# Optimization experiments

Hardware: AMD Instinct MI355X
Metric: run time of the kernel (lower is better)

## Reference

```python
import jax, jax.numpy as jnp
import numpy as np

N = 100000      # number of vertices
E = 3200000     # number of directed edges (avg degree 32)
EPS = 1e-8
WEIGHT = 0.01


def setup_inputs() -> dict:
    key = jax.random.key(0)
    k1, k2, k3, k4 = jax.random.split(key, 4)
    mu0 = jax.random.normal(k1, (N, 3), dtype=jnp.float32)
    # current positions = canonical + small deformation (realistic ARAP setting)
    mu = mu0 + 0.1 * jax.random.normal(k2, (N, 3), dtype=jnp.float32)
    i = jax.random.randint(k3, (E,), 0, N, dtype=jnp.int32)
    # avoid self-edges (rest length 0 would give w = 1/eps = 1e8 and swamp the loss)
    off = jax.random.randint(k4, (E,), 1, N, dtype=jnp.int32)
    j = (i + off) % N
    edge_idx = jnp.stack([i, j], axis=0)  # (2, E)
    return {"mu0": mu0, "mu": mu, "edge_idx": edge_idx}


def reference(mu0, mu, edge_idx):
    i, j = edge_idx[0], edge_idx[1]
    rest = mu0[j] - mu0[i]        # (E,3) canonical edge vectors
    deform = mu[j] - mu[i]        # (E,3) deformed edge vectors
    w = 1.0 / (jnp.linalg.norm(rest, axis=-1) + EPS)  # (E,)
    # per-edge weighted outer product deform \otimes rest
    outer = jnp.einsum('e,ei,ej->eij', w, deform, rest)  # (E,3,3)
    # scatter-add into per-node covariance matrices
    S = jnp.zeros((mu0.shape[0], 3, 3), dtype=mu0.dtype).at[i].add(outer)  # (N,3,3)
    U, _, Vh = jnp.linalg.svd(S, full_matrices=False)
    R = U @ Vh
    det_mask = (jnp.linalg.det(R) < 0)[:, None, None]
    diag_fix = jnp.array([-1.0, 1.0, 1.0], dtype=mu0.dtype).reshape(1, 1, 3)
    Vh = jnp.where(det_mask, Vh * diag_fix, Vh)
    R = U @ Vh                      # (N,3,3) best-fit rotations
    Ri = R[i]                       # (E,3,3)
    pred = jnp.einsum('eij,ej->ei', Ri, rest)
    err = deform - pred
    loss = jnp.sum(w * jnp.sum(err * err, axis=-1)) / jnp.sum(w)
    return WEIGHT * loss
```

## Files before the change

kernel.cpp:

```cpp
#include <hip/hip_runtime.h>
#include <hip/hip_fp16.h>
#include <math.h>

#define EPS     1e-8f
#define MP      131
#define JBITS   17
#define JMASK   ((1u << JBITS) - 1u)
#define CAP     6144
#define PMAX    1024
#define ACC_T   576
#define MAXPT   11
#define BIN_T   512
#define CHUNK   8192
#define EPT     16

struct alignas(16) Pk { __half2 a, b, c; unsigned pad; };

__global__ __launch_bounds__(256) void k_prep(
    const float* __restrict__ mu0, const float* __restrict__ mu,
    Pk* __restrict__ pk, int* __restrict__ gcursor, int N, int P)
{
    int n = blockIdx.x * blockDim.x + threadIdx.x;
    if (n < P) gcursor[n] = n * CAP;
    if (n >= N) return;
    float x0 = mu0[3*n+0], y0 = mu0[3*n+1], z0 = mu0[3*n+2];
    float x1 = mu [3*n+0], y1 = mu [3*n+1], z1 = mu [3*n+2];
    Pk o;
    o.a = __floats2half2_rn(x0, y0);
    o.b = __floats2half2_rn(z0, x1);
    o.c = __floats2half2_rn(y1, z1);
    o.pad = 0u;
    pk[n] = o;
}

__global__ __launch_bounds__(BIN_T) void k_bin(
    const int* __restrict__ ei, const int* __restrict__ ej,
    int* __restrict__ gcursor, unsigned* __restrict__ bucket,
    int E, int P)
{
    __shared__ int cnt[PMAX];
    __shared__ int dbase[PMAX];
    __shared__ int scan_tmp[PMAX];
    __shared__ unsigned sortw[CHUNK];
    __shared__ unsigned short sortp[CHUNK];

    int lo = blockIdx.x * CHUNK;
    int hi = lo + CHUNK; if (hi > E) hi = E;
    int ce = hi - lo;
    int tid = threadIdx.x;

    for (int t = tid; t < PMAX; t += BIN_T) cnt[t] = 0;

    int myi[EPT], myj[EPT];
    #pragma unroll
    for (int k = 0; k < EPT; ++k) {
        int e = lo + tid + k * BIN_T;
        if (e < hi) {
            myi[k] = __builtin_nontemporal_load(&ei[e]);
            myj[k] = __builtin_nontemporal_load(&ej[e]);
        } else myi[k] = -1;
    }
    __syncthreads();

    #pragma unroll
    for (int k = 0; k < EPT; ++k)
        if (myi[k] >= 0) atomicAdd(&cnt[(unsigned)myi[k] / (unsigned)MP], 1);
    __syncthreads();

    {
        int t1 = tid + BIN_T;
        scan_tmp[tid] = cnt[tid];
        scan_tmp[t1]  = cnt[t1];
        __syncthreads();
        for (int off = 1; off < PMAX; off <<= 1) {
            int a0 = (tid >= off) ? scan_tmp[tid - off] : 0;
            int a1 = scan_tmp[t1 - off];
            __syncthreads();
            scan_tmp[tid] += a0;
            scan_tmp[t1]  += a1;
            __syncthreads();
        }
    }

    for (int t = tid; t < P; t += BIN_T) {
        int c = cnt[t];
        int excl = scan_tmp[t] - c;
        int b = c ? atomicAdd(&gcursor[t], c) : 0;
        dbase[t] = b - excl;
        cnt[t] = excl;
    }
    __syncthreads();

    #pragma unroll
    for (int k = 0; k < EPT; ++k) {
        if (myi[k] >= 0) {
            int i = myi[k];
            int p = (int)((unsigned)i / (unsigned)MP);
            int li = i - p * MP;
            int pos = atomicAdd(&cnt[p], 1);
            sortw[pos] = ((unsigned)li << JBITS) | (unsigned)myj[k];
            sortp[pos] = (unsigned short)p;
        }
    }
    __syncthreads();

    for (int s = tid; s < ce; s += BIN_T) {
        unsigned w = sortw[s];
        int p = sortp[s];
        int dst = dbase[p] + s;
        if (dst < (p + 1) * CAP)
            bucket[dst] = w;
    }
}

__global__ __launch_bounds__(ACC_T) void k_accum(
    const Pk* __restrict__ pk,
    const unsigned* __restrict__ bucket, const int* __restrict__ gcursor,
    double* __restrict__ pblk, int N)
{
    __shared__ unsigned sorted[CAP];
    __shared__ int hist[MP];
    __shared__ int offs[MP];
    __shared__ int cursor[MP];
    __shared__ int sc[192];
    __shared__ float Sl[MP * 9];
    __shared__ double redw[9], rede[9];

    int p = blockIdx.x;
    int lo_n = p * MP;
    int beg = p * CAP;
    int end = gcursor[p];
    int cap_end = beg + CAP;
    if (end > cap_end) end = cap_end;

    for (int t = threadIdx.x; t < MP; t += ACC_T) hist[t] = 0;
    __syncthreads();

    unsigned myu[MAXPT];
    int mycnt = 0;
    {
        int e = beg + threadIdx.x;
        #pragma unroll
        for (int k = 0; k < MAXPT; ++k) {
            if (e < end) {
                unsigned uu = bucket[e];
                myu[k] = uu;
                atomicAdd(&hist[uu >> JBITS], 1);
                ++mycnt;
            }
            e += ACC_T;
        }
    }
    __syncthreads();

    if (threadIdx.x < 192) {
        int v = (threadIdx.x < MP) ? hist[threadIdx.x] : 0;
        int incl = v;
        #pragma unroll
        for (int d = 1; d < 64; d <<= 1) {
            int o = __shfl_up(incl, d);
            if ((threadIdx.x & 63) >= d) incl += o;
        }
        sc[threadIdx.x] = incl;
    }
    __syncthreads();
    if (threadIdx.x < MP) {
        int w = threadIdx.x >> 6;
        int carry = 0;
        if (w >= 1) carry += sc[63];
        if (w >= 2) carry += sc[127];
        int excl = sc[threadIdx.x] - hist[threadIdx.x] + carry;
        offs[threadIdx.x] = excl;
        cursor[threadIdx.x] = excl;
    }
    __syncthreads();

    #pragma unroll
    for (int k = 0; k < MAXPT; ++k) {
        if (k < mycnt) {
            unsigned uu = myu[k];
            int li = (int)(uu >> JBITS);
            int pos = atomicAdd(&cursor[li], 1);
            sorted[pos] = uu;
        }
    }
    __syncthreads();

    double wsum = 0.0, errsum = 0.0;
    float S[9] = {0.f,0.f,0.f,0.f,0.f,0.f,0.f,0.f,0.f};
    {
        int node = threadIdx.x >> 2;
        int part = threadIdx.x & 3;
        int n = lo_n + node;
        if (node < MP && n < N) {
            Pk ac = pk[n];
            float2 a01 = __half22float2(ac.a);
            float2 a23 = __half22float2(ac.b);
            float2 a45 = __half22float2(ac.c);
            float ax = a01.x, ay = a01.y, az = a23.x;
            float cx = a23.y, cy = a45.x, cz = a45.y;

            auto body = [&](const Pk& cc) {
                float2 f01 = __half22float2(cc.a);
                float2 f23 = __half22float2(cc.b);
                float2 f45 = __half22float2(cc.c);
                float r0 = f01.x - ax, r1 = f01.y - ay, r2 = f23.x - az;
                float d0 = f23.y - cx, d1 = f45.x - cy, d2 = f45.y - cz;
                float rr = r0*r0 + r1*r1 + r2*r2;
                float dd = d0*d0 + d1*d1 + d2*d2;
                float w  = 1.0f / (sqrtf(rr) + EPS);
                wsum   += (double)w;
                errsum += (double)(w * (dd + rr));
                float wd0 = w*d0, wd1 = w*d1, wd2 = w*d2;
                S[0] += wd0*r0; S[1] += wd0*r1; S[2] += wd0*r2;
                S[3] += wd1*r0; S[4] += wd1*r1; S[5] += wd1*r2;
                S[6] += wd2*r0; S[7] += wd2*r1; S[8] += wd2*r2;
            };

            int b0 = offs[node];
            int e1 = b0 + hist[node];
            int e  = b0 + part;
            for (; e + 4 < e1; e += 8) {
                unsigned u0 = sorted[e], u1 = sorted[e + 4];
                Pk c0 = pk[u0 & JMASK];
                Pk c1 = pk[u1 & JMASK];
                body(c0);
                body(c1);
            }
            if (e < e1) {
                Pk c0 = pk[sorted[e] & JMASK];
                body(c0);
            }
        }
        #pragma unroll
        for (int c = 0; c < 9; ++c) {
            S[c] += __shfl_down(S[c], 2);
            S[c] += __shfl_down(S[c], 1);
        }
        if (part == 0 && node < MP)
            #pragma unroll
            for (int c = 0; c < 9; ++c) Sl[node*9 + c] = S[c];
    }
    __syncthreads();

    if (threadIdx.x < MP && lo_n + (int)threadIdx.x < N) {
        float Sf[9], X[9];
        #pragma unroll
        for (int c = 0; c < 9; ++c) { Sf[c] = Sl[threadIdx.x*9 + c]; X[c] = Sf[c]; }
        bool ok = true;
        #pragma unroll
        for (int it = 0; it < 8; ++it) {
            float c00 =  (X[4]*X[8] - X[5]*X[7]);
            float c01 = -(X[3]*X[8] - X[5]*X[6]);
            float c02 =  (X[3]*X[7] - X[4]*X[6]);
            float c10 = -(X[1]*X[8] - X[2]*X[7]);
            float c11 =  (X[0]*X[8] - X[2]*X[6]);
            float c12 = -(X[0]*X[7] - X[1]*X[6]);
            float c20 =  (X[1]*X[5] - X[2]*X[4]);
            float c21 = -(X[0]*X[5] - X[2]*X[3]);
            float c22 =  (X[0]*X[4] - X[1]*X[3]);
            float det = X[0]*c00 + X[1]*c01 + X[2]*c02;
            if (!(fabsf(det) > 1e-30f)) { ok = false; break; }
            float inv_det = 1.0f / det;
            float Y[9] = { c00*inv_det, c01*inv_det, c02*inv_det,
                           c10*inv_det, c11*inv_det, c12*inv_det,
                           c20*inv_det, c21*inv_det, c22*inv_det };
            float nx = 0.f, ny = 0.f;
            #pragma unroll
            for (int c = 0; c < 9; ++c) { nx += X[c]*X[c]; ny += Y[c]*Y[c]; }
            float g = sqrtf(sqrtf(ny / nx));
            float hg = 0.5f * g, hig = 0.5f / g;
            #pragma unroll
            for (int c = 0; c < 9; ++c) X[c] = hg * X[c] + hig * Y[c];
        }
        if (!ok) {
            X[0]=1.f; X[1]=0.f; X[2]=0.f;
            X[3]=0.f; X[4]=1.f; X[5]=0.f;
            X[6]=0.f; X[7]=0.f; X[8]=1.f;
        }
        float det = X[0]*(X[4]*X[8] - X[5]*X[7])
                  - X[1]*(X[3]*X[8] - X[5]*X[6])
                  + X[2]*(X[3]*X[7] - X[4]*X[6]);
        if (det < 0.f) { X[0] = -X[0]; X[3] = -X[3]; X[6] = -X[6]; }
        float tr = X[0]*Sf[0] + X[1]*Sf[1] + X[2]*Sf[2]
                 + X[3]*Sf[3] + X[4]*Sf[4] + X[5]*Sf[5]
                 + X[6]*Sf[6] + X[7]*Sf[7] + X[8]*Sf[8];
        errsum -= 2.0 * (double)tr;
    }

    #pragma unroll
    for (int off = 32; off > 0; off >>= 1) {
        wsum   += __shfl_down(wsum, off);
        errsum += __shfl_down(errsum, off);
    }
    if ((threadIdx.x & 63) == 0) {
        redw[threadIdx.x >> 6] = wsum;
        rede[threadIdx.x >> 6] = errsum;
    }
    __syncthreads();
    if (threadIdx.x == 0) {
        double W = 0.0, Er = 0.0;
        #pragma unroll
        for (int k = 0; k < 9; ++k) { W += redw[k]; Er += rede[k]; }
        pblk[2*p]   = W;
        pblk[2*p+1] = Er;
    }
}

__global__ __launch_bounds__(256) void k_final(
    const double* __restrict__ pblk, int nb, float* __restrict__ out)
{
    __shared__ double sw[4], se[4];
    double w = 0.0, e = 0.0;
    for (int t = threadIdx.x; t < nb; t += 256) {
        w += pblk[2*t];
        e += pblk[2*t+1];
    }
    #pragma unroll
    for (int off = 32; off > 0; off >>= 1) {
        w += __shfl_down(w, off);
        e += __shfl_down(e, off);
    }
    if ((threadIdx.x & 63) == 0) {
        sw[threadIdx.x >> 6] = w;
        se[threadIdx.x >> 6] = e;
    }
    __syncthreads();
    if (threadIdx.x == 0) {
        double W  = sw[0] + sw[1] + sw[2] + sw[3];
        double Er = se[0] + se[1] + se[2] + se[3];
        out[0] = (float)(0.01 * (Er / W));
    }
}

extern "C" void kernel_launch(void* const* d_in, const int* in_sizes, int n_in,
                              void* d_out, int out_size, void* d_ws, size_t ws_size,
                              hipStream_t stream) {
    const float* mu0 = (const float*)d_in[0];
    const float* mu  = (const float*)d_in[1];
    const int*   eidx = (const int*)d_in[2];
    int N = in_sizes[0] / 3;
    int E = in_sizes[2] / 2;
    const int* ei = eidx;
    const int* ej = eidx + E;

    int P = (N + MP - 1) / MP;

    double*   pblk    = (double*)d_ws;
    int*      gcursor = (int*)((char*)d_ws + 2 * PMAX * sizeof(double));
    Pk*       pk      = (Pk*)((char*)d_ws + 2 * PMAX * sizeof(double) + PMAX * sizeof(int));
    unsigned* bucket  = (unsigned*)(pk + N);

    int nbin = (E + CHUNK - 1) / CHUNK;

    k_prep  <<<(N + 255) / 256, 256, 0, stream>>>(mu0, mu, pk, gcursor, N, P);
    k_bin   <<<nbin, BIN_T, 0, stream>>>(ei, ej, gcursor, bucket, E, P);
    k_accum <<<P, ACC_T, 0, stream>>>(pk, bucket, gcursor, pblk, N);
    k_final <<<1, 256, 0, stream>>>(pblk, P, (float*)d_out);
}
```

Before: 129.3 us.

## Fuse prep into binning kernel and shard bucket cursors to reduce atomic contention

The node-packing prep kernel is folded into the binning kernel, so each bin block also packs a slice of nodes, and the cursors are zeroed with a memset instead of a kernel. Each partition's bucket region is split into two half-capacity shards chosen by block parity. The shard cursors are padded apart so global atomics on the same partition contend less and do not share cache lines. The accumulate kernel then reads the two shard runs separately. Each shard is capped at half capacity, so a skewed partition could overflow one shard and drop edges that the old single region would have held.

```diff
diff --git a/kernel.cpp b/kernel.cpp
--- a/kernel.cpp
+++ b/kernel.cpp
@@ -7,36 +7,23 @@
 #define JBITS   17
 #define JMASK   ((1u << JBITS) - 1u)
 #define CAP     6144
+#define HCAP    3072
 #define PMAX    1024
+#define GPAD    32
 #define ACC_T   576
-#define MAXPT   11
+#define MRUN    6
 #define BIN_T   512
 #define CHUNK   8192
 #define EPT     16
 
 struct alignas(16) Pk { __half2 a, b, c; unsigned pad; };
 
-__global__ __launch_bounds__(256) void k_prep(
+__global__ __launch_bounds__(BIN_T) void k_bin(
     const float* __restrict__ mu0, const float* __restrict__ mu,
-    Pk* __restrict__ pk, int* __restrict__ gcursor, int N, int P)
-{
-    int n = blockIdx.x * blockDim.x + threadIdx.x;
-    if (n < P) gcursor[n] = n * CAP;
-    if (n >= N) return;
-    float x0 = mu0[3*n+0], y0 = mu0[3*n+1], z0 = mu0[3*n+2];
-    float x1 = mu [3*n+0], y1 = mu [3*n+1], z1 = mu [3*n+2];
-    Pk o;
-    o.a = __floats2half2_rn(x0, y0);
-    o.b = __floats2half2_rn(z0, x1);
-    o.c = __floats2half2_rn(y1, z1);
-    o.pad = 0u;
-    pk[n] = o;
-}
-
-__global__ __launch_bounds__(BIN_T) void k_bin(
+    Pk* __restrict__ pk,
     const int* __restrict__ ei, const int* __restrict__ ej,
     int* __restrict__ gcursor, unsigned* __restrict__ bucket,
-    int E, int P)
+    int E, int N, int P, int nper)
 {
     __shared__ int cnt[PMAX];
     __shared__ int dbase[PMAX];
@@ -44,10 +31,31 @@
     __shared__ unsigned sortw[CHUNK];
     __shared__ unsigned short sortp[CHUNK];
 
+    int tid = threadIdx.x;
+
+    {
+        int n0 = blockIdx.x * nper;
+        int n1 = n0 + nper; if (n1 > N) n1 = N;
+        for (int n = n0 + tid; n < n1; n += BIN_T) {
+            float x0 = __builtin_nontemporal_load(&mu0[3*n+0]);
+            float y0 = __builtin_nontemporal_load(&mu0[3*n+1]);
+            float z0 = __builtin_nontemporal_load(&mu0[3*n+2]);
+            float x1 = __builtin_nontemporal_load(&mu [3*n+0]);
+            float y1 = __builtin_nontemporal_load(&mu [3*n+1]);
+            float z1 = __builtin_nontemporal_load(&mu [3*n+2]);
+            Pk o;
+            o.a = __floats2half2_rn(x0, y0);
+            o.b = __floats2half2_rn(z0, x1);
+            o.c = __floats2half2_rn(y1, z1);
+            o.pad = 0u;
+            pk[n] = o;
+        }
+    }
+
     int lo = blockIdx.x * CHUNK;
     int hi = lo + CHUNK; if (hi > E) hi = E;
     int ce = hi - lo;
-    int tid = threadIdx.x;
+    int shard = blockIdx.x & 1;
 
     for (int t = tid; t < PMAX; t += BIN_T) cnt[t] = 0;
 
@@ -85,8 +93,8 @@
     for (int t = tid; t < P; t += BIN_T) {
         int c = cnt[t];
         int excl = scan_tmp[t] - c;
-        int b = c ? atomicAdd(&gcursor[t], c) : 0;
-        dbase[t] = b - excl;
+        int b = c ? atomicAdd(&gcursor[(2*t + shard) * GPAD], c) : 0;
+        dbase[t] = t * CAP + shard * HCAP + b - excl;
         cnt[t] = excl;
     }
     __syncthreads();
@@ -104,11 +112,12 @@
     }
     __syncthreads();
 
+    int slim = shard * HCAP + HCAP;
     for (int s = tid; s < ce; s += BIN_T) {
         unsigned w = sortw[s];
         int p = sortp[s];
         int dst = dbase[p] + s;
-        if (dst < (p + 1) * CAP)
+        if (dst < p * CAP + slim)
             bucket[dst] = w;
     }
 }
@@ -128,27 +137,34 @@
 
     int p = blockIdx.x;
     int lo_n = p * MP;
-    int beg = p * CAP;
-    int end = gcursor[p];
-    int cap_end = beg + CAP;
-    if (end > cap_end) end = cap_end;
+    int c0 = gcursor[(2*p    ) * GPAD]; if (c0 > HCAP) c0 = HCAP;
+    int c1 = gcursor[(2*p + 1) * GPAD]; if (c1 > HCAP) c1 = HCAP;
+    int beg0 = p * CAP;
+    int beg1 = p * CAP + HCAP;
 
     for (int t = threadIdx.x; t < MP; t += ACC_T) hist[t] = 0;
     __syncthreads();
 
-    unsigned myu[MAXPT];
-    int mycnt = 0;
-    {
-        int e = beg + threadIdx.x;
-        #pragma unroll
-        for (int k = 0; k < MAXPT; ++k) {
-            if (e < end) {
-                unsigned uu = bucket[e];
-                myu[k] = uu;
-                atomicAdd(&hist[uu >> JBITS], 1);
-                ++mycnt;
-            }
-            e += ACC_T;
+    unsigned myu0[MRUN], myu1[MRUN];
+    int v0 = 0, v1 = 0;
+    #pragma unroll
+    for (int k = 0; k < MRUN; ++k) {
+        int e = beg0 + threadIdx.x + k * ACC_T;
+        if (e < beg0 + c0) {
+            unsigned uu = bucket[e];
+            myu0[k] = uu;
+            atomicAdd(&hist[uu >> JBITS], 1);
+            ++v0;
+        }
+    }
+    #pragma unroll
+    for (int k = 0; k < MRUN; ++k) {
+        int e = beg1 + threadIdx.x + k * ACC_T;
+        if (e < beg1 + c1) {
+            unsigned uu = bucket[e];
+            myu1[k] = uu;
+            atomicAdd(&hist[uu >> JBITS], 1);
+            ++v1;
         }
     }
     __syncthreads();
@@ -176,11 +192,18 @@
     __syncthreads();
 
     #pragma unroll
-    for (int k = 0; k < MAXPT; ++k) {
-        if (k < mycnt) {
-            unsigned uu = myu[k];
-            int li = (int)(uu >> JBITS);
-            int pos = atomicAdd(&cursor[li], 1);
+    for (int k = 0; k < MRUN; ++k) {
+        if (k < v0) {
+            unsigned uu = myu0[k];
+            int pos = atomicAdd(&cursor[uu >> JBITS], 1);
+            sorted[pos] = uu;
+        }
+    }
+    #pragma unroll
+    for (int k = 0; k < MRUN; ++k) {
+        if (k < v1) {
+            unsigned uu = myu1[k];
+            int pos = atomicAdd(&cursor[uu >> JBITS], 1);
             sorted[pos] = uu;
         }
     }
@@ -222,14 +245,14 @@
             int e  = b0 + part;
             for (; e + 4 < e1; e += 8) {
                 unsigned u0 = sorted[e], u1 = sorted[e + 4];
-                Pk c0 = pk[u0 & JMASK];
-                Pk c1 = pk[u1 & JMASK];
-                body(c0);
-                body(c1);
+                Pk cc0 = pk[u0 & JMASK];
+                Pk cc1 = pk[u1 & JMASK];
+                body(cc0);
+                body(cc1);
             }
             if (e < e1) {
-                Pk c0 = pk[sorted[e] & JMASK];
-                body(c0);
+                Pk cc0 = pk[sorted[e] & JMASK];
+                body(cc0);
             }
         }
         #pragma unroll
@@ -348,13 +371,16 @@
 
     double*   pblk    = (double*)d_ws;
     int*      gcursor = (int*)((char*)d_ws + 2 * PMAX * sizeof(double));
-    Pk*       pk      = (Pk*)((char*)d_ws + 2 * PMAX * sizeof(double) + PMAX * sizeof(int));
+    Pk*       pk      = (Pk*)((char*)d_ws + 2 * PMAX * sizeof(double)
+                                          + 2 * PMAX * GPAD * sizeof(int));
     unsigned* bucket  = (unsigned*)(pk + N);
 
     int nbin = (E + CHUNK - 1) / CHUNK;
-
-    k_prep  <<<(N + 255) / 256, 256, 0, stream>>>(mu0, mu, pk, gcursor, N, P);
-    k_bin   <<<nbin, BIN_T, 0, stream>>>(ei, ej, gcursor, bucket, E, P);
+    int nper = (N + nbin - 1) / nbin;
+
+    hipMemsetAsync(gcursor, 0, 2 * PMAX * GPAD * sizeof(int), stream);
+    k_bin   <<<nbin, BIN_T, 0, stream>>>(mu0, mu, pk, ei, ej, gcursor, bucket,
+                                         E, N, P, nper);
     k_accum <<<P, ACC_T, 0, stream>>>(pk, bucket, gcursor, pblk, N);
     k_final <<<1, 256, 0, stream>>>(pblk, P, (float*)d_out);
 }
```

After: 132.0 us. 2.1% more time.

## Balance edge accumulation by splitting sorted edge range evenly across threads

Applied to the files above, without the earlier changes.

Replaces the fixed four-threads-per-node assignment with a flat split of the block's sorted edge list, giving each thread a contiguous equal-sized segment. Partial covariance sums are flushed to shared memory with atomic adds whenever the owning node changes, which requires zero-initialising the shared accumulator. This removes load imbalance from varying node degrees and the idle threads left over by the node mapping. In exchange it adds shared-memory float atomics, a reload of the anchor node data at each segment boundary, and a more branchy inner loop.

```diff
diff --git a/kernel.cpp b/kernel.cpp
--- a/kernel.cpp
+++ b/kernel.cpp
@@ -134,6 +134,7 @@
     if (end > cap_end) end = cap_end;
 
     for (int t = threadIdx.x; t < MP; t += ACC_T) hist[t] = 0;
+    for (int t = threadIdx.x; t < MP * 9; t += ACC_T) Sl[t] = 0.f;
     __syncthreads();
 
     unsigned myu[MAXPT];
@@ -187,59 +188,54 @@
     __syncthreads();
 
     double wsum = 0.0, errsum = 0.0;
-    float S[9] = {0.f,0.f,0.f,0.f,0.f,0.f,0.f,0.f,0.f};
     {
-        int node = threadIdx.x >> 2;
-        int part = threadIdx.x & 3;
-        int n = lo_n + node;
-        if (node < MP && n < N) {
-            Pk ac = pk[n];
-            float2 a01 = __half22float2(ac.a);
-            float2 a23 = __half22float2(ac.b);
-            float2 a45 = __half22float2(ac.c);
-            float ax = a01.x, ay = a01.y, az = a23.x;
-            float cx = a23.y, cy = a45.x, cz = a45.y;
-
-            auto body = [&](const Pk& cc) {
-                float2 f01 = __half22float2(cc.a);
-                float2 f23 = __half22float2(cc.b);
-                float2 f45 = __half22float2(cc.c);
-                float r0 = f01.x - ax, r1 = f01.y - ay, r2 = f23.x - az;
-                float d0 = f23.y - cx, d1 = f45.x - cy, d2 = f45.y - cz;
-                float rr = r0*r0 + r1*r1 + r2*r2;
-                float dd = d0*d0 + d1*d1 + d2*d2;
-                float w  = 1.0f / (sqrtf(rr) + EPS);
-                wsum   += (double)w;
-                errsum += (double)(w * (dd + rr));
-                float wd0 = w*d0, wd1 = w*d1, wd2 = w*d2;
-                S[0] += wd0*r0; S[1] += wd0*r1; S[2] += wd0*r2;
-                S[3] += wd1*r0; S[4] += wd1*r1; S[5] += wd1*r2;
-                S[6] += wd2*r0; S[7] += wd2*r1; S[8] += wd2*r2;
-            };
-
-            int b0 = offs[node];
-            int e1 = b0 + hist[node];
-            int e  = b0 + part;
-            for (; e + 4 < e1; e += 8) {
-                unsigned u0 = sorted[e], u1 = sorted[e + 4];
-                Pk c0 = pk[u0 & JMASK];
-                Pk c1 = pk[u1 & JMASK];
-                body(c0);
-                body(c1);
+        int tot = end - beg;
+        int q = (tot + ACC_T - 1) / ACC_T;
+        int s0 = threadIdx.x * q;
+        int s1 = s0 + q; if (s1 > tot) s1 = tot;
+        float S[9] = {0.f,0.f,0.f,0.f,0.f,0.f,0.f,0.f,0.f};
+        int cur = -1;
+        float ax=0.f, ay=0.f, az=0.f, cx=0.f, cy=0.f, cz=0.f;
+        for (int s = s0; s < s1; ++s) {
+            unsigned uu = sorted[s];
+            Pk cc = pk[uu & JMASK];
+            int li = (int)(uu >> JBITS);
+            if (li != cur) {
+                if (cur >= 0) {
+                    float* b = Sl + cur * 9;
+                    #pragma unroll
+                    for (int c = 0; c < 9; ++c) atomicAdd(b + c, S[c]);
+                    #pragma unroll
+                    for (int c = 0; c < 9; ++c) S[c] = 0.f;
+                }
+                cur = li;
+                Pk ac = pk[lo_n + li];
+                float2 a01 = __half22float2(ac.a);
+                float2 a23 = __half22float2(ac.b);
+                float2 a45 = __half22float2(ac.c);
+                ax = a01.x; ay = a01.y; az = a23.x;
+                cx = a23.y; cy = a45.x; cz = a45.y;
             }
-            if (e < e1) {
-                Pk c0 = pk[sorted[e] & JMASK];
-                body(c0);
-            }
-        }
-        #pragma unroll
-        for (int c = 0; c < 9; ++c) {
-            S[c] += __shfl_down(S[c], 2);
-            S[c] += __shfl_down(S[c], 1);
-        }
-        if (part == 0 && node < MP)
+            float2 f01 = __half22float2(cc.a);
+            float2 f23 = __half22float2(cc.b);
+            float2 f45 = __half22float2(cc.c);
+            float r0 = f01.x - ax, r1 = f01.y - ay, r2 = f23.x - az;
+            float d0 = f23.y - cx, d1 = f45.x - cy, d2 = f45.y - cz;
+            float rr = r0*r0 + r1*r1 + r2*r2;
+            float dd = d0*d0 + d1*d1 + d2*d2;
+            float w  = 1.0f / (sqrtf(rr) + EPS);
+            wsum   += (double)w;
+            errsum += (double)(w * (dd + rr));
+            float wd0 = w*d0, wd1 = w*d1, wd2 = w*d2;
+            S[0] += wd0*r0; S[1] += wd0*r1; S[2] += wd0*r2;
+            S[3] += wd1*r0; S[4] += wd1*r1; S[5] += wd1*r2;
+            S[6] += wd2*r0; S[7] += wd2*r1; S[8] += wd2*r2;
+        }
+        if (cur >= 0) {
+            float* b = Sl + cur * 9;
             #pragma unroll
-            for (int c = 0; c < 9; ++c) Sl[node*9 + c] = S[c];
+            for (int c = 0; c < 9; ++c) atomicAdd(b + c, S[c]);
+        }
     }
     __syncthreads();
 
```

After: 146.0 us. 1.13x slower.
